# Optimization experiments

Measured on AMD Instinct MI355X. Metric: run time of the kernel, lower is better.

The kernel has to match this reference:

```python
import jax, jax.numpy as jnp
import numpy as np

M = 8192   # predicted boxes
N = 8192   # ground-truth boxes
W_CENTER, W_SIZE, W_IOU = 1.0, 0.5, 2.0
MATCH_THRESH = 5.0


def setup_inputs() -> dict:
    key = jax.random.key(0)
    k1, k2, k3, k4 = jax.random.split(key, 4)
    centers = jax.random.uniform(k1, (N, 3), dtype=jnp.float32) * 100.0
    sizes = jax.random.uniform(k2, (N, 3), dtype=jnp.float32) * 3.0 + 1.0
    yaw = jax.random.uniform(k3, (N, 1), dtype=jnp.float32) * (2.0 * jnp.pi) - jnp.pi
    gt_boxes = jnp.concatenate([centers, sizes, yaw], axis=1)  # [N,7]
    # preds = perturbed gts so the 5.0 m matching gate actually fires
    pred_boxes = gt_boxes + 0.5 * jax.random.normal(k4, (M, 7), dtype=jnp.float32)
    return {"pred_boxes": pred_boxes, "gt_boxes": gt_boxes}


def _greedy_match(pred_boxes, gt_boxes):
    """Sequential greedy nearest-center matching (torch loop -> lax.scan).
    Column deletion in the original is equivalent to masking with an
    availability vector: argmin over remaining columns with first-tie wins.
    Returns (mask [M] bool: pred i matched, idx [M] int: matched gt index)."""
    # [M,N] center distance matrix (the memory-heavy irregular part)
    diff = pred_boxes[:, None, :3] - gt_boxes[None, :, :3]
    dist = jnp.sqrt(jnp.sum(diff * diff, axis=-1))

    def step(avail, d_row):
        dm = jnp.where(avail, d_row, jnp.inf)
        j = jnp.argmin(dm)
        ok = dm[j] < MATCH_THRESH
        avail = avail.at[j].set(jnp.logical_and(avail[j], jnp.logical_not(ok)))
        return avail, (ok, j)

    avail0 = jnp.ones((gt_boxes.shape[0],), dtype=bool)
    _, (mask, idx) = jax.lax.scan(step, avail0, dist)
    return mask, idx


def _smooth_l1(x):
    a = jnp.abs(x)
    return jnp.where(a < 1.0, 0.5 * a * a, a - 0.5)


def _iou_2d(b1, b2):
    # axis-aligned BEV IoU using (x, y, l, w)
    x1, y1, l1, w1 = b1[:, 0], b1[:, 1], b1[:, 3], b1[:, 4]
    x2, y2, l2, w2 = b2[:, 0], b2[:, 1], b2[:, 3], b2[:, 4]
    iw = jnp.clip(jnp.minimum(x1 + l1 / 2, x2 + l2 / 2) - jnp.maximum(x1 - l1 / 2, x2 - l2 / 2), 0.0)
    ih = jnp.clip(jnp.minimum(y1 + w1 / 2, y2 + w2 / 2) - jnp.maximum(y1 - w1 / 2, y2 - w2 / 2), 0.0)
    inter = iw * ih
    union = l1 * w1 + l2 * w2 - inter
    return inter / (union + 1e-6)


def _loss(pred_boxes, gt_boxes, mask, idx):
    mg = gt_boxes[idx]                              # [M,7] matched gts
    m = mask.astype(pred_boxes.dtype)               # [M]
    k = jnp.maximum(jnp.sum(m), 1.0)                # number of matches
    loss_center = jnp.sum(m[:, None] * _smooth_l1(pred_boxes[:, :3] - mg[:, :3])) / (3.0 * k)
    loss_size = jnp.sum(m[:, None] * _smooth_l1(pred_boxes[:, 3:6] - mg[:, 3:6])) / (3.0 * k)
    d = pred_boxes[:, 6] - mg[:, 6]
    d = jnp.arctan2(jnp.sin(d), jnp.cos(d))         # wrap to (-pi, pi]
    loss_orient = jnp.sum(m * _smooth_l1(d)) / k
    loss_iou = jnp.sum(m * (1.0 - _iou_2d(pred_boxes, mg))) / k
    return W_CENTER * loss_center + W_SIZE * (loss_size + loss_orient) + W_IOU * loss_iou


def reference(pred_boxes, gt_boxes):
    mask, idx = _greedy_match(pred_boxes, gt_boxes)
    return _loss(pred_boxes, gt_boxes, mask, idx)
```

## Files before the change

kernel.cpp:

```cpp
#include <hip/hip_runtime.h>
#include <stdint.h>

#define MROWS 8192
#define NGT   8192
#define KC    8
#define KL    4
#define RPW   2
#define THRESH_BITS 0x40A00000u

__device__ __forceinline__ unsigned dist_bits(float px, float py, float pz,
                                              float gx, float gy, float gz) {
#pragma clang fp contract(off)
  float dx = px - gx;
  float dy = py - gy;
  float dz = pz - gz;
  float s = (dx * dx + dy * dy) + dz * dz;
  return __float_as_uint(sqrtf(s));
}

__device__ __forceinline__ unsigned long long wave_min64(unsigned long long v) {
#pragma unroll
  for (int off = 32; off >= 1; off >>= 1) {
    unsigned long long o = __shfl_xor(v, off, 64);
    v = (o < v) ? o : v;
  }
  return v;
}

template <int K>
__device__ __forceinline__ void insert_sorted(unsigned (&kd)[K], unsigned (&ki)[K],
                                              unsigned key, unsigned j) {
#pragma unroll
  for (int t = K - 1; t >= 1; --t) {
    bool a = key < kd[t];
    bool b = key < kd[t - 1];
    if (a) {
      if (b) { kd[t] = kd[t - 1]; ki[t] = ki[t - 1]; }
      else   { kd[t] = key;       ki[t] = j; }
    }
  }
  if (key < kd[0]) { kd[0] = key; ki[0] = j; }
}

template <int K>
__device__ __forceinline__ void extract8(unsigned (&kd)[K], unsigned (&ki)[K], int lane,
                                         unsigned& resd, unsigned& resi,
                                         unsigned long long& e8) {
#pragma unroll
  for (int rr = 0; rr < KC; ++rr) {
    unsigned long long head = ((unsigned long long)kd[0] << 32) | (unsigned long long)ki[0];
    unsigned long long m = wave_min64(head);
    if (head == m) {
#pragma unroll
      for (int t = 0; t < K - 1; ++t) { kd[t] = kd[t + 1]; ki[t] = ki[t + 1]; }
      kd[K - 1] = 0xFFFFFFFFu; ki[K - 1] = 0xFFFFFFFFu;
    }
    if (lane == rr) { resd = (unsigned)(m >> 32); resi = (unsigned)m; }
    e8 = m;
  }
}

__global__ __launch_bounds__(256) void pack_kernel(const float* __restrict__ gt,
                                                   float4* __restrict__ cen) {
  int j = blockIdx.x * 256 + threadIdx.x;
  if (j < NGT) cen[j] = make_float4(gt[j * 7 + 0], gt[j * 7 + 1], gt[j * 7 + 2], 0.0f);
}

__global__ __launch_bounds__(256, 4) void topk_kernel(const float* __restrict__ pred,
                                                      const float4* __restrict__ cen,
                                                      uint2* __restrict__ cand) {
  const int tid = threadIdx.x;
  const int lane = tid & 63;
  const int wave = (blockIdx.x * 256 + tid) >> 6;
  const int r0 = wave * RPW;

  float px[RPW], py[RPW], pz[RPW];
#pragma unroll
  for (int r = 0; r < RPW; ++r) {
    px[r] = pred[(size_t)(r0 + r) * 7 + 0];
    py[r] = pred[(size_t)(r0 + r) * 7 + 1];
    pz[r] = pred[(size_t)(r0 + r) * 7 + 2];
  }

  unsigned kd[RPW][KL], ki[RPW][KL];
#pragma unroll
  for (int r = 0; r < RPW; ++r)
#pragma unroll
    for (int t = 0; t < KL; ++t) { kd[r][t] = 0xFFFFFFFFu; ki[r][t] = 0xFFFFFFFFu; }

#pragma unroll 2
  for (int j0 = 0; j0 < NGT / 64; ++j0) {
    int j = j0 * 64 + lane;
    float4 c = cen[j];
#pragma unroll
    for (int r = 0; r < RPW; ++r) {
      unsigned key = dist_bits(px[r], py[r], pz[r], c.x, c.y, c.z);
      if (key < kd[r][KL - 1]) insert_sorted<KL>(kd[r], ki[r], key, (unsigned)j);
    }
  }

#pragma unroll
  for (int r = 0; r < RPW; ++r) {
    const int row = r0 + r;
    unsigned long long guard =
        ((unsigned long long)kd[r][KL - 1] << 32) | (unsigned long long)ki[r][KL - 1];
    unsigned resd = 0, resi = 0;
    unsigned long long e8 = 0;
    extract8<KL>(kd[r], ki[r], lane, resd, resi, e8);

    if (__ballot(guard < e8) != 0ull) {
      unsigned fd[KC], fi[KC];
#pragma unroll
      for (int t = 0; t < KC; ++t) { fd[t] = 0xFFFFFFFFu; fi[t] = 0xFFFFFFFFu; }
      for (int j0 = 0; j0 < NGT / 64; ++j0) {
        int j = j0 * 64 + lane;
        float4 c = cen[j];
        unsigned key = dist_bits(px[r], py[r], pz[r], c.x, c.y, c.z);
        if (key < fd[KC - 1]) insert_sorted<KC>(fd, fi, key, (unsigned)j);
      }
      unsigned long long dummy;
      extract8<KC>(fd, fi, lane, resd, resi, dummy);
    }
    if (lane < KC) cand[(size_t)row * KC + lane] = make_uint2(resd, resi);
  }
}

__device__ __forceinline__ void load_cand_row(const uint2* __restrict__ cand, int row,
                                              unsigned (&dd)[KC], unsigned (&ii)[KC]) {
  const uint4* cr = (const uint4*)(cand + (size_t)row * KC);
#pragma unroll
  for (int q = 0; q < 4; ++q) {
    uint4 v = cr[q];
    dd[q * 2 + 0] = v.x; ii[q * 2 + 0] = v.y;
    dd[q * 2 + 1] = v.z; ii[q * 2 + 1] = v.w;
  }
}

__global__ __launch_bounds__(64) void greedy_kernel(const uint2* __restrict__ cand,
                                                    const float* __restrict__ pred,
                                                    const float* __restrict__ gt,
                                                    unsigned* __restrict__ match) {
  __shared__ unsigned avail[NGT / 32];
  __shared__ unsigned claim[NGT];
  __shared__ float sx[NGT], sy[NGT], sz[NGT];
  const int lane = threadIdx.x;

  for (int w = lane; w < NGT / 32; w += 64) avail[w] = 0xFFFFFFFFu;
  for (int j = lane; j < NGT; j += 64) {
    claim[j] = 0xFFFFFFFFu;
    sx[j] = gt[j * 7 + 0];
    sy[j] = gt[j * 7 + 1];
    sz[j] = gt[j * 7 + 2];
  }
  __syncthreads();

  unsigned cd[KC], ci[KC], nd[KC], ni[KC];
  int prefBase = -1;

  int base = 0;
  while (base < MROWS) {
    const int nAct = (MROWS - base < 64) ? (MROWS - base) : 64;
    const int row = base + lane;
    const bool active = lane < nAct;

    if (base == prefBase) {
#pragma unroll
      for (int t = 0; t < KC; ++t) { cd[t] = nd[t]; ci[t] = ni[t]; }
    } else {
      load_cand_row(cand, active ? row : (MROWS - 1), cd, ci);
    }
    prefBase = base + nAct;
    {
      int pr = prefBase + lane;
      if (pr >= MROWS) pr = MROWS - 1;
      load_cand_row(cand, pr, nd, ni);
    }

    unsigned m = 0;
#pragma unroll
    for (int t = 0; t < KC; ++t) {
      unsigned g = ci[t];
      m |= ((avail[g >> 5] >> (g & 31)) & 1u) << t;
    }
    if (!active) m = 0;

    unsigned pd = 0xFFFFFFFFu, pg = 0u;
    bool isClaim = false;
    bool forceSerial = false;
    int guard = 0;
    while (true) {
      pd = 0xFFFFFFFFu; pg = 0u;
#pragma unroll
      for (int t = KC - 1; t >= 0; --t)
        if (m & (1u << t)) { pd = cd[t]; pg = ci[t]; }
      isClaim = active && (m != 0u) && (pd < THRESH_BITS);
      if (isClaim) atomicMin(&claim[pg], (unsigned)lane);
      __builtin_amdgcn_wave_barrier();
      bool lost = isClaim && (claim[pg] < (unsigned)lane);
      unsigned long long adv = __ballot(lost);
      if (adv == 0ull) break;
      if (lost) m &= (m - 1u);
      if (++guard > 600) { forceSerial = true; break; }
    }

    unsigned long long exb = __ballot(active && (m == 0u));
    int firstExh = exb ? (__ffsll(exb) - 1) : 64;
    if (forceSerial) firstExh = 0;
    int commitCount = firstExh < nAct ? firstExh : nAct;

    if (active && lane < commitCount) {
      match[row] = (isClaim ? 0x80000000u : 0u) | pg;
      if (isClaim) atomicAnd(&avail[pg >> 5], ~(1u << (pg & 31)));
    }
#pragma unroll
    for (int t = 0; t < KC; ++t) claim[ci[t]] = 0xFFFFFFFFu;
    __builtin_amdgcn_wave_barrier();

    base += commitCount;

    if (commitCount < nAct) {
      const int r = base;
      float fx = pred[(size_t)r * 7 + 0];
      float fy = pred[(size_t)r * 7 + 1];
      float fz = pred[(size_t)r * 7 + 2];
      unsigned long long best = ~0ull;
      for (int j0 = 0; j0 < NGT / 64; ++j0) {
        int j = j0 * 64 + lane;
        if ((avail[j >> 5] >> (j & 31)) & 1u) {
          unsigned db = dist_bits(fx, fy, fz, sx[j], sy[j], sz[j]);
          unsigned long long key = ((unsigned long long)db << 32) | (unsigned)j;
          if (key < best) best = key;
        }
      }
      unsigned long long mm = wave_min64(best);
      if (lane == 0) {
        if (mm == ~0ull) {
          match[r] = 0u;
        } else {
          unsigned db = (unsigned)(mm >> 32);
          unsigned j = (unsigned)mm;
          bool ok = db < THRESH_BITS;
          if (ok) atomicAnd(&avail[j >> 5], ~(1u << (j & 31)));
          match[r] = (ok ? 0x80000000u : 0u) | j;
        }
      }
      __builtin_amdgcn_wave_barrier();
      base += 1;
    }
  }
}

__device__ __forceinline__ float smooth_l1(float x) {
  float a = fabsf(x);
  return (a < 1.0f) ? (0.5f * a * a) : (a - 0.5f);
}

__global__ __launch_bounds__(256) void loss_kernel(const float* __restrict__ pred,
                                                   const float* __restrict__ gt,
                                                   const unsigned* __restrict__ match,
                                                   float* __restrict__ acc) {
  int i = blockIdx.x * 256 + threadIdx.x;
  float vc = 0.f, vs = 0.f, vo = 0.f, vi = 0.f, vk = 0.f;
  if (i < MROWS) {
    unsigned r = match[i];
    if (r & 0x80000000u) {
      unsigned j = r & 0x7FFFFFFFu;
      float p[7], g[7];
#pragma unroll
      for (int t = 0; t < 7; ++t) { p[t] = pred[i * 7 + t]; g[t] = gt[j * 7 + t]; }
      vc = smooth_l1(p[0] - g[0]) + smooth_l1(p[1] - g[1]) + smooth_l1(p[2] - g[2]);
      vs = smooth_l1(p[3] - g[3]) + smooth_l1(p[4] - g[4]) + smooth_l1(p[5] - g[5]);
      float d = p[6] - g[6];
      float w = d - 6.283185307179586f * rintf(d * 0.15915494309189535f);
      vo = smooth_l1(w);
      float iw = fminf(p[0] + p[3] * 0.5f, g[0] + g[3] * 0.5f) -
                 fmaxf(p[0] - p[3] * 0.5f, g[0] - g[3] * 0.5f);
      iw = fmaxf(iw, 0.0f);
      float ih = fminf(p[1] + p[4] * 0.5f, g[1] + g[4] * 0.5f) -
                 fmaxf(p[1] - p[4] * 0.5f, g[1] - g[4] * 0.5f);
      ih = fmaxf(ih, 0.0f);
      float inter = iw * ih;
      float uni = p[3] * p[4] + g[3] * g[4] - inter;
      vi = 1.0f - inter / (uni + 1e-6f);
      vk = 1.0f;
    }
  }
#pragma unroll
  for (int off = 32; off >= 1; off >>= 1) {
    vc += __shfl_down(vc, off, 64);
    vs += __shfl_down(vs, off, 64);
    vo += __shfl_down(vo, off, 64);
    vi += __shfl_down(vi, off, 64);
    vk += __shfl_down(vk, off, 64);
  }
  if ((threadIdx.x & 63) == 0) {
    atomicAdd(&acc[0], vc);
    atomicAdd(&acc[1], vs);
    atomicAdd(&acc[2], vo);
    atomicAdd(&acc[3], vi);
    atomicAdd(&acc[4], vk);
  }
}

__global__ void finalize_kernel(const float* __restrict__ acc, float* __restrict__ out) {
  float k = fmaxf(acc[4], 1.0f);
  float loss = acc[0] / (3.0f * k)
             + 0.5f * (acc[1] / (3.0f * k) + acc[2] / k)
             + 2.0f * (acc[3] / k);
  out[0] = loss;
}

extern "C" void kernel_launch(void* const* d_in, const int* in_sizes, int n_in,
                              void* d_out, int out_size, void* d_ws, size_t ws_size,
                              hipStream_t stream) {
  const float* pred = (const float*)d_in[0];
  const float* gt   = (const float*)d_in[1];
  char* ws = (char*)d_ws;
  float* acc       = (float*)ws;
  unsigned* match  = (unsigned*)(ws + 1024);
  uint2* cand      = (uint2*)(ws + 33792);
  float4* cen      = (float4*)(ws + 558080);

  hipMemsetAsync(acc, 0, 32, stream);
  pack_kernel<<<NGT / 256, 256, 0, stream>>>(gt, cen);
  topk_kernel<<<MROWS / (RPW * 4), 256, 0, stream>>>(pred, cen, cand);
  greedy_kernel<<<1, 64, 0, stream>>>(cand, pred, gt, match);
  loss_kernel<<<MROWS / 256, 256, 0, stream>>>(pred, gt, match, acc);
  finalize_kernel<<<1, 1, 0, stream>>>(acc, (float*)d_out);
}
```

Baseline: 236.3 us.

## Process four rows per lane in greedy matcher with compact candidate encoding

The single-wave greedy matcher now handles up to 256 rows per round (four per lane) instead of 64, so fewer serial rounds are needed. Candidate entries are packed into one word holding the gt index and a below-threshold bit, which halves candidate bandwidth. The top-k pass also compares squared distances and skips the sqrt. In exchange each lane keeps more registers, conflicts are more likely within a round, and the threshold test now relies on a squared-distance bit constant matching the sqrt comparison.

```diff
diff --git a/kernel.cpp b/kernel.cpp
--- a/kernel.cpp
+++ b/kernel.cpp
@@ -6,16 +6,18 @@
 #define KC    8
 #define KL    4
 #define RPW   2
-#define THRESH_BITS 0x40A00000u
-
-__device__ __forceinline__ unsigned dist_bits(float px, float py, float pz,
-                                              float gx, float gy, float gz) {
+#define RPL   4
+#define THRESH2_BITS 0x41C7FFFFu
+#define THRESH_BITS  0x40A00000u
+
+__device__ __forceinline__ unsigned dist2_bits(float px, float py, float pz,
+                                               float gx, float gy, float gz) {
 #pragma clang fp contract(off)
   float dx = px - gx;
   float dy = py - gy;
   float dz = pz - gz;
   float s = (dx * dx + dy * dy) + dz * dz;
-  return __float_as_uint(sqrtf(s));
+  return __float_as_uint(s);
 }
 
 __device__ __forceinline__ unsigned long long wave_min64(unsigned long long v) {
@@ -68,7 +70,7 @@
 
 __global__ __launch_bounds__(256, 4) void topk_kernel(const float* __restrict__ pred,
                                                       const float4* __restrict__ cen,
-                                                      uint2* __restrict__ cand) {
+                                                      unsigned* __restrict__ cand) {
   const int tid = threadIdx.x;
   const int lane = tid & 63;
   const int wave = (blockIdx.x * 256 + tid) >> 6;
@@ -94,7 +96,7 @@
     float4 c = cen[j];
 #pragma unroll
     for (int r = 0; r < RPW; ++r) {
-      unsigned key = dist_bits(px[r], py[r], pz[r], c.x, c.y, c.z);
+      unsigned key = dist2_bits(px[r], py[r], pz[r], c.x, c.y, c.z);
       if (key < kd[r][KL - 1]) insert_sorted<KL>(kd[r], ki[r], key, (unsigned)j);
     }
   }
@@ -115,28 +117,18 @@
       for (int j0 = 0; j0 < NGT / 64; ++j0) {
         int j = j0 * 64 + lane;
         float4 c = cen[j];
-        unsigned key = dist_bits(px[r], py[r], pz[r], c.x, c.y, c.z);
+        unsigned key = dist2_bits(px[r], py[r], pz[r], c.x, c.y, c.z);
         if (key < fd[KC - 1]) insert_sorted<KC>(fd, fi, key, (unsigned)j);
       }
       unsigned long long dummy;
       extract8<KC>(fd, fi, lane, resd, resi, dummy);
     }
-    if (lane < KC) cand[(size_t)row * KC + lane] = make_uint2(resd, resi);
-  }
-}
-
-__device__ __forceinline__ void load_cand_row(const uint2* __restrict__ cand, int row,
-                                              unsigned (&dd)[KC], unsigned (&ii)[KC]) {
-  const uint4* cr = (const uint4*)(cand + (size_t)row * KC);
-#pragma unroll
-  for (int q = 0; q < 4; ++q) {
-    uint4 v = cr[q];
-    dd[q * 2 + 0] = v.x; ii[q * 2 + 0] = v.y;
-    dd[q * 2 + 1] = v.z; ii[q * 2 + 1] = v.w;
-  }
-}
-
-__global__ __launch_bounds__(64) void greedy_kernel(const uint2* __restrict__ cand,
+    if (lane < KC)
+      cand[(size_t)row * KC + lane] = (resi << 1) | (resd < THRESH2_BITS ? 1u : 0u);
+  }
+}
+
+__global__ __launch_bounds__(64) void greedy_kernel(const unsigned* __restrict__ cand,
                                                     const float* __restrict__ pred,
                                                     const float* __restrict__ gt,
                                                     unsigned* __restrict__ match) {
@@ -154,66 +146,111 @@
   }
   __syncthreads();
 
-  unsigned cd[KC], ci[KC], nd[KC], ni[KC];
+  unsigned ci_[RPL][KC], ni_[RPL][KC];
   int prefBase = -1;
 
   int base = 0;
   while (base < MROWS) {
-    const int nAct = (MROWS - base < 64) ? (MROWS - base) : 64;
-    const int row = base + lane;
-    const bool active = lane < nAct;
+    const int nAct = (MROWS - base < 64 * RPL) ? (MROWS - base) : 64 * RPL;
 
     if (base == prefBase) {
 #pragma unroll
-      for (int t = 0; t < KC; ++t) { cd[t] = nd[t]; ci[t] = ni[t]; }
+      for (int q = 0; q < RPL; ++q)
+#pragma unroll
+        for (int t = 0; t < KC; ++t) ci_[q][t] = ni_[q][t];
     } else {
-      load_cand_row(cand, active ? row : (MROWS - 1), cd, ci);
+#pragma unroll
+      for (int q = 0; q < RPL; ++q) {
+        int o = lane + 64 * q;
+        int r = base + (o < nAct ? o : 0);
+        const uint4* cr = (const uint4*)(cand + (size_t)r * KC);
+        uint4 a = cr[0], b = cr[1];
+        ci_[q][0] = a.x; ci_[q][1] = a.y; ci_[q][2] = a.z; ci_[q][3] = a.w;
+        ci_[q][4] = b.x; ci_[q][5] = b.y; ci_[q][6] = b.z; ci_[q][7] = b.w;
+      }
     }
     prefBase = base + nAct;
-    {
-      int pr = prefBase + lane;
+#pragma unroll
+    for (int q = 0; q < RPL; ++q) {
+      int pr = prefBase + lane + 64 * q;
       if (pr >= MROWS) pr = MROWS - 1;
-      load_cand_row(cand, pr, nd, ni);
-    }
-
-    unsigned m = 0;
-#pragma unroll
-    for (int t = 0; t < KC; ++t) {
-      unsigned g = ci[t];
-      m |= ((avail[g >> 5] >> (g & 31)) & 1u) << t;
-    }
-    if (!active) m = 0;
-
-    unsigned pd = 0xFFFFFFFFu, pg = 0u;
-    bool isClaim = false;
+      const uint4* cr = (const uint4*)(cand + (size_t)pr * KC);
+      uint4 a = cr[0], b = cr[1];
+      ni_[q][0] = a.x; ni_[q][1] = a.y; ni_[q][2] = a.z; ni_[q][3] = a.w;
+      ni_[q][4] = b.x; ni_[q][5] = b.y; ni_[q][6] = b.z; ni_[q][7] = b.w;
+    }
+
+    unsigned m[RPL];
+#pragma unroll
+    for (int q = 0; q < RPL; ++q) {
+      int o = lane + 64 * q;
+      unsigned mm = 0;
+#pragma unroll
+      for (int t = 0; t < KC; ++t) {
+        unsigned g = ci_[q][t] >> 1;
+        mm |= ((avail[g >> 5] >> (g & 31)) & 1u) << t;
+      }
+      m[q] = (o < nAct) ? mm : 0u;
+    }
+
+    unsigned pe[RPL];
+    bool cl[RPL];
     bool forceSerial = false;
     int guard = 0;
     while (true) {
-      pd = 0xFFFFFFFFu; pg = 0u;
-#pragma unroll
-      for (int t = KC - 1; t >= 0; --t)
-        if (m & (1u << t)) { pd = cd[t]; pg = ci[t]; }
-      isClaim = active && (m != 0u) && (pd < THRESH_BITS);
-      if (isClaim) atomicMin(&claim[pg], (unsigned)lane);
+#pragma unroll
+      for (int q = 0; q < RPL; ++q) {
+        unsigned e = 0;
+#pragma unroll
+        for (int t = KC - 1; t >= 0; --t)
+          if (m[q] & (1u << t)) e = ci_[q][t];
+        pe[q] = e;
+        cl[q] = (m[q] != 0u) && (e & 1u);
+      }
+#pragma unroll
+      for (int q = 0; q < RPL; ++q)
+        if (cl[q]) atomicMin(&claim[pe[q] >> 1], (unsigned)(lane + 64 * q));
       __builtin_amdgcn_wave_barrier();
-      bool lost = isClaim && (claim[pg] < (unsigned)lane);
-      unsigned long long adv = __ballot(lost);
-      if (adv == 0ull) break;
-      if (lost) m &= (m - 1u);
-      if (++guard > 600) { forceSerial = true; break; }
-    }
-
-    unsigned long long exb = __ballot(active && (m == 0u));
-    int firstExh = exb ? (__ffsll(exb) - 1) : 64;
-    if (forceSerial) firstExh = 0;
-    int commitCount = firstExh < nAct ? firstExh : nAct;
-
-    if (active && lane < commitCount) {
-      match[row] = (isClaim ? 0x80000000u : 0u) | pg;
-      if (isClaim) atomicAnd(&avail[pg >> 5], ~(1u << (pg & 31)));
-    }
-#pragma unroll
-    for (int t = 0; t < KC; ++t) claim[ci[t]] = 0xFFFFFFFFu;
+      bool any = false;
+      bool lost[RPL];
+#pragma unroll
+      for (int q = 0; q < RPL; ++q) {
+        lost[q] = cl[q] && (claim[pe[q] >> 1] < (unsigned)(lane + 64 * q));
+        any |= lost[q];
+      }
+      if (__ballot(any) == 0ull) break;
+#pragma unroll
+      for (int q = 0; q < RPL; ++q)
+        if (lost[q]) m[q] &= (m[q] - 1u);
+      if (++guard > 2100) { forceSerial = true; break; }
+    }
+
+    unsigned fe = 1024u;
+#pragma unroll
+    for (int q = 0; q < RPL; ++q) {
+      unsigned o = (unsigned)(lane + 64 * q);
+      if (o < (unsigned)nAct && m[q] == 0u && o < fe) fe = o;
+    }
+#pragma unroll
+    for (int off = 32; off >= 1; off >>= 1) {
+      unsigned other = __shfl_xor(fe, off, 64);
+      fe = other < fe ? other : fe;
+    }
+    int commitCount = forceSerial ? 0 : ((int)fe < nAct ? (int)fe : nAct);
+
+#pragma unroll
+    for (int q = 0; q < RPL; ++q) {
+      int o = lane + 64 * q;
+      if (o < commitCount) {
+        unsigned g = pe[q] >> 1;
+        match[base + o] = (cl[q] ? 0x80000000u : 0u) | g;
+        if (cl[q]) atomicAnd(&avail[g >> 5], ~(1u << (g & 31)));
+      }
+    }
+#pragma unroll
+    for (int q = 0; q < RPL; ++q)
+#pragma unroll
+      for (int t = 0; t < KC; ++t) claim[ci_[q][t] >> 1] = 0xFFFFFFFFu;
     __builtin_amdgcn_wave_barrier();
 
     base += commitCount;
@@ -227,18 +264,26 @@
       for (int j0 = 0; j0 < NGT / 64; ++j0) {
         int j = j0 * 64 + lane;
         if ((avail[j >> 5] >> (j & 31)) & 1u) {
-          unsigned db = dist_bits(fx, fy, fz, sx[j], sy[j], sz[j]);
+          unsigned db;
+          {
+#pragma clang fp contract(off)
+            float dx = fx - sx[j];
+            float dy = fy - sy[j];
+            float dz = fz - sz[j];
+            float s = (dx * dx + dy * dy) + dz * dz;
+            db = __float_as_uint(sqrtf(s));
+          }
           unsigned long long key = ((unsigned long long)db << 32) | (unsigned)j;
           if (key < best) best = key;
         }
       }
-      unsigned long long mm = wave_min64(best);
+      unsigned long long mm2 = wave_min64(best);
       if (lane == 0) {
-        if (mm == ~0ull) {
+        if (mm2 == ~0ull) {
           match[r] = 0u;
         } else {
-          unsigned db = (unsigned)(mm >> 32);
-          unsigned j = (unsigned)mm;
+          unsigned db = (unsigned)(mm2 >> 32);
+          unsigned j = (unsigned)mm2;
           bool ok = db < THRESH_BITS;
           if (ok) atomicAnd(&avail[j >> 5], ~(1u << (j & 31)));
           match[r] = (ok ? 0x80000000u : 0u) | j;
@@ -318,8 +363,8 @@
   char* ws = (char*)d_ws;
   float* acc       = (float*)ws;
   unsigned* match  = (unsigned*)(ws + 1024);
-  uint2* cand      = (uint2*)(ws + 33792);
-  float4* cen      = (float4*)(ws + 558080);
+  unsigned* cand   = (unsigned*)(ws + 33792);
+  float4* cen      = (float4*)(ws + 295936);
 
   hipMemsetAsync(acc, 0, 32, stream);
   pack_kernel<<<NGT / 256, 256, 0, stream>>>(gt, cen);
```

Result: faster. 214.9 us (-9.0%).
